# Kernel tuning notes

Measured on AMD Instinct MI355X. Metric: run time of the kernel, lower is better.

## Reference

```python
import jax, jax.numpy as jnp
import numpy as np
import math

B, C, H, W = 32, 3, 512, 512
K = 16
OUT_H, OUT_W = 512, 512

def _ctrl_pts(k):
    gs = int(math.sqrt(k))
    lin = jnp.linspace(-1.0, 1.0, gs)
    gy, gx = jnp.meshgrid(lin, lin, indexing='ij')
    return jnp.stack([gx, gy], axis=-1).reshape(-1, 2)

def setup_inputs() -> dict:
    key = jax.random.key(0)
    k1, k2, k3, k4 = jax.random.split(key, 4)
    x = jax.random.normal(k1, (B, C, H, W), jnp.float32)
    conv_w = jax.random.normal(k2, (8, C, 7, 7), jnp.float32) * 0.05
    conv_b = jax.random.normal(k3, (8,), jnp.float32) * 0.05
    fc_w = jax.random.normal(k4, (2 * K, 8), jnp.float32) * 0.01
    fc_b = jnp.asarray(_ctrl_pts(K).reshape(-1))  # module inits bias to ctrl grid
    return {"x": x, "conv_w": conv_w, "conv_b": conv_b, "fc_w": fc_w, "fc_b": fc_b}

def _U(sq):
    # U(r) = r^2 * log(r^2 + 1e-6), expressed with squared distance sq = r^2
    return sq * jnp.log(sq + 1e-6)

def _tps_grid(src, tgt, out_h, out_w):
    # src: [K,2] shared across batch (fixed ctrl grid), tgt: [B,K,2]
    Bb, Kk, _ = tgt.shape
    lin_y = jnp.linspace(-1.0, 1.0, out_h)
    lin_x = jnp.linspace(-1.0, 1.0, out_w)
    gy, gx = jnp.meshgrid(lin_y, lin_x, indexing='ij')
    grid = jnp.stack([gx, gy], axis=-1).reshape(-1, 2)  # [N,2]
    N = out_h * out_w
    # RBF kernel between output grid and source ctrl pts: [N,K]
    d2 = jnp.sum((grid[:, None, :] - src[None, :, :]) ** 2, axis=-1)
    U = _U(d2)
    # TPS system matrix L [K+3,K+3]; src is batch-shared so build it once
    src_d2 = jnp.sum((src[:, None, :] - src[None, :, :]) ** 2, axis=-1)
    P = jnp.concatenate([jnp.ones((Kk, 1)), src], axis=1)  # [K,3]
    L = jnp.zeros((Kk + 3, Kk + 3))
    L = L.at[:Kk, :Kk].set(_U(src_d2))
    L = L.at[:Kk, Kk:].set(P)
    L = L.at[Kk:, :Kk].set(P.T)
    Y = jnp.concatenate([tgt, jnp.zeros((Bb, 3, 2))], axis=1)  # [B,K+3,2]
    Wmat = jnp.linalg.solve(L[None], Y)  # [B,K+3,2]
    Pg = jnp.concatenate([jnp.ones((N, 1)), grid], axis=1)  # [N,3]
    mapped = (jnp.einsum('nk,bkc->bnc', U, Wmat[:, :Kk])
              + jnp.einsum('np,bpc->bnc', Pg, Wmat[:, Kk:]))
    return mapped.reshape(Bb, out_h, out_w, 2)

def _grid_sample(x, grid):
    # bilinear, zero padding, align_corners=False (torch defaults)
    Bb, Cc, Hh, Ww = x.shape
    ix = ((grid[..., 0] + 1.0) * Ww - 1.0) * 0.5
    iy = ((grid[..., 1] + 1.0) * Hh - 1.0) * 0.5
    x0 = jnp.floor(ix)
    y0 = jnp.floor(iy)
    wx1 = ix - x0
    wy1 = iy - y0
    x0i = x0.astype(jnp.int32)
    y0i = y0.astype(jnp.int32)

    def gather(img, yy, xx):
        valid = ((yy >= 0) & (yy < Hh) & (xx >= 0) & (xx < Ww)).astype(img.dtype)
        yc = jnp.clip(yy, 0, Hh - 1)
        xc = jnp.clip(xx, 0, Ww - 1)
        return img[:, yc, xc] * valid[None]

    def per(img, x0i, y0i, wx1, wy1):
        wx0 = 1.0 - wx1
        wy0 = 1.0 - wy1
        v00 = gather(img, y0i, x0i)
        v01 = gather(img, y0i, x0i + 1)
        v10 = gather(img, y0i + 1, x0i)
        v11 = gather(img, y0i + 1, x0i + 1)
        return (v00 * (wy0 * wx0)[None] + v01 * (wy0 * wx1)[None]
                + v10 * (wy1 * wx0)[None] + v11 * (wy1 * wx1)[None])

    return jax.vmap(per)(x, x0i, y0i, wx1, wy1)

def reference(x, conv_w, conv_b, fc_w, fc_b):
    # localization: conv7x7 -> relu -> global avg pool -> fc
    feat = jax.lax.conv_general_dilated(
        x, conv_w, window_strides=(1, 1), padding='VALID',
        dimension_numbers=('NCHW', 'OIHW', 'NCHW'))
    feat = jax.nn.relu(feat + conv_b[None, :, None, None])
    pooled = feat.mean(axis=(2, 3))  # [B,8] (AdaptiveAvgPool2d(1))
    pred = (pooled @ fc_w.T + fc_b).reshape(-1, K, 2)  # [B,K,2]
    src = _ctrl_pts(K)
    grid = _tps_grid(src, pred, OUT_H, OUT_W)  # [B,OUT_H,OUT_W,2]
    return _grid_sample(x, grid)
```

## Files before the change

kernel.cpp:

```cpp
#include <hip/hip_runtime.h>
#include <hip/hip_bf16.h>
#include <hip/hip_fp16.h>
#include <math.h>

#define BATCH 32
#define CH_IN 3
#define CH_OUT 8
#define IMG 512
#define KSZ 7
#define CONV_OUT 506
#define KPTS 16
#define TILES_PER_B 128

#define SROWS 23
#define PITCH_DW 76
#define SMEM_DW (CH_IN * SROWS * PITCH_DW)

#define BPB 8

typedef _Float16 half8_t __attribute__((ext_vector_type(8)));
typedef float f32x4_t __attribute__((ext_vector_type(4)));

__device__ __forceinline__ unsigned short f2h_bits(float f) {
    _Float16 h = (_Float16)f;
    unsigned short u;
    __builtin_memcpy(&u, &h, 2);
    return u;
}
__device__ __forceinline__ float h2f_bits(unsigned short u) {
    _Float16 h;
    __builtin_memcpy(&h, &u, 2);
    return (float)h;
}

__global__ __launch_bounds__(256)
void h16_kernel(const float* __restrict__ x, unsigned int* __restrict__ xh) {
    const int total4 = BATCH * CH_IN * IMG * IMG / 4;
    int stride = gridDim.x * 256;
    for (int p = blockIdx.x * 256 + threadIdx.x; p < total4; p += stride) {
        float4 v = ((const float4*)x)[p];
        unsigned int lo = (unsigned int)f2h_bits(v.x) | ((unsigned int)f2h_bits(v.y) << 16);
        unsigned int hi = (unsigned int)f2h_bits(v.z) | ((unsigned int)f2h_bits(v.w) << 16);
        xh[2 * p] = lo;
        xh[2 * p + 1] = hi;
    }
}

__global__ void wprep_kernel(const float* __restrict__ w, uint4* __restrict__ afrag) {
    int idx = blockIdx.x * 256 + threadIdx.x;
    if (idx >= 6 * 64) return;
    int s = idx >> 6, l = idx & 63;
    int m = l & 15;
    int dlt = m >> 3, o = m & 7;
    int oct = s * 4 + (l >> 4);
    int c = oct >> 3, ky = oct & 7;
    unsigned short h[8];
    #pragma unroll
    for (int j = 0; j < 8; ++j) {
        int kx = j - dlt;
        float v = 0.f;
        if (ky < KSZ && kx >= 0 && kx < KSZ)
            v = w[((o * CH_IN + c) * KSZ + ky) * KSZ + kx];
        h[j] = f2h_bits(v);
    }
    uint4 out;
    __builtin_memcpy(&out, h, 16);
    afrag[idx] = out;
}

template <bool H16>
__global__ __launch_bounds__(256)
void conv_pool_kernel(const float* __restrict__ x, const unsigned short* __restrict__ xh,
                      const uint4* __restrict__ afrag, const float* __restrict__ conv_b,
                      float* __restrict__ partial) {
    __shared__ unsigned int smem[SMEM_DW];
    __shared__ float red[4][8];

    int blk = blockIdx.x;
    int b = blk >> 7;
    int stripe = (blk >> 2) & 31;
    int chunk = blk & 3;
    int ybase = stripe * 16;
    int x0 = chunk * 128;
    int tid = threadIdx.x;

    if (H16) {
        const unsigned short* xhb = xh + (size_t)b * CH_IN * IMG * IMG;
        for (int idx4 = tid; idx4 < SMEM_DW / 4; idx4 += 256) {
            int c = idx4 / (SROWS * 19);
            int rem = idx4 - c * (SROWS * 19);
            int r = rem / 19;
            int u4 = rem - r * 19;
            int grow = ybase + r;
            int gcol = x0 + (u4 << 3);
            uint4 v = make_uint4(0u, 0u, 0u, 0u);
            if (grow < IMG) {
                const unsigned short* rp = xhb + ((size_t)c * IMG + grow) * IMG;
                if (gcol + 8 <= IMG) {
                    v = *(const uint4*)(rp + gcol);
                } else {
                    unsigned short h[8] = {0, 0, 0, 0, 0, 0, 0, 0};
                    #pragma unroll
                    for (int j = 0; j < 8; ++j) {
                        int cc = gcol + j;
                        if (cc < IMG) h[j] = rp[cc];
                    }
                    __builtin_memcpy(&v, h, 16);
                }
            }
            ((uint4*)smem)[idx4] = v;
        }
    } else {
        for (int idx = tid; idx < SMEM_DW; idx += 256) {
            int c = idx / (SROWS * PITCH_DW);
            int rem = idx - c * (SROWS * PITCH_DW);
            int r = rem / PITCH_DW;
            int u = rem - r * PITCH_DW;
            int grow = ybase + r, gcol = x0 + 2 * u;
            float f0 = 0.f, f1 = 0.f;
            if (grow < IMG) {
                const float* rp = x + (((size_t)b * CH_IN + c) * IMG + grow) * IMG;
                if (gcol < IMG) f0 = rp[gcol];
                if (gcol + 1 < IMG) f1 = rp[gcol + 1];
            }
            smem[idx] = (unsigned int)f2h_bits(f0) | ((unsigned int)f2h_bits(f1) << 16);
        }
    }
    __syncthreads();

    int l = tid & 63, w = tid >> 6;
    int n = l & 15, g = l >> 4;

    uint4 at[6];
    #pragma unroll
    for (int s = 0; s < 6; ++s) at[s] = afrag[s * 64 + l];

    int rowb[6];
    #pragma unroll
    for (int s = 0; s < 6; ++s) {
        int oct = s * 4 + g;
        int c = oct >> 3, ky = oct & 7;
        rowb[s] = (c * SROWS + n + ky) * (PITCH_DW * 4) + w * 64;
    }

    float bias_[4];
    {
        int ob = (g & 1) * 4;
        #pragma unroll
        for (int r2 = 0; r2 < 4; ++r2) bias_[r2] = conv_b[ob + r2];
    }
    bool rowok = (ybase + n) < CONV_OUT;
    int dlt = g >> 1;
    float sums[4] = {0.f, 0.f, 0.f, 0.f};
    const char* sb = (const char*)smem;

    #pragma unroll
    for (int u = 0; u < 4; ++u) {
        f32x4_t acc[4];
        #pragma unroll
        for (int d = 0; d < 4; ++d) acc[d] = (f32x4_t){0.f, 0.f, 0.f, 0.f};

        #pragma unroll
        for (int s = 0; s < 6; ++s) {
            uint4 lo = *(const uint4*)(sb + rowb[s] + (u << 4));
            uint4 hi = *(const uint4*)(sb + rowb[s] + (u << 4) + 16);
            unsigned int eu[8] = {lo.x, lo.y, lo.z, lo.w, hi.x, hi.y, hi.z, hi.w};
            half8_t a;
            __builtin_memcpy(&a, &at[s], 16);
            #pragma unroll
            for (int d = 0; d < 4; ++d) {
                uint4 bu = make_uint4(eu[d], eu[d + 1], eu[d + 2], eu[d + 3]);
                half8_t bf;
                __builtin_memcpy(&bf, &bu, 16);
                acc[d] = __builtin_amdgcn_mfma_f32_16x16x32_f16(a, bf, acc[d], 0, 0, 0);
            }
        }

        #pragma unroll
        for (int d = 0; d < 4; ++d) {
            int col = x0 + 32 * w + 8 * u + 2 * d + dlt;
            bool colok = col < CONV_OUT;
            #pragma unroll
            for (int r2 = 0; r2 < 4; ++r2) {
                float v = acc[d][r2] + bias_[r2];
                v = v > 0.f ? v : 0.f;
                sums[r2] += (rowok && colok) ? v : 0.f;
            }
        }
    }

    #pragma unroll
    for (int r2 = 0; r2 < 4; ++r2) {
        sums[r2] += __shfl_xor(sums[r2], 1, 64);
        sums[r2] += __shfl_xor(sums[r2], 2, 64);
        sums[r2] += __shfl_xor(sums[r2], 4, 64);
        sums[r2] += __shfl_xor(sums[r2], 8, 64);
        sums[r2] += __shfl_xor(sums[r2], 32, 64);
    }
    if (l == 0) {
        #pragma unroll
        for (int r2 = 0; r2 < 4; ++r2) red[w][r2] = sums[r2];
    }
    if (l == 16) {
        #pragma unroll
        for (int r2 = 0; r2 < 4; ++r2) red[w][4 + r2] = sums[r2];
    }
    __syncthreads();
    if (tid < CH_OUT) {
        float s = red[0][tid] + red[1][tid] + red[2][tid] + red[3][tid];
        partial[(b * TILES_PER_B + stripe * 4 + chunk) * CH_OUT + tid] = s;
    }
}

__device__ __forceinline__ double ctrl_lin(int i) { return -1.0 + (2.0 / 3.0) * i; }

__global__ void solve_kernel(const float* __restrict__ partial,
                             const float* __restrict__ fc_w,
                             const float* __restrict__ fc_b,
                             float* __restrict__ Wf) {
    __shared__ double L[19][19];
    __shared__ double Ys[19][64];
    __shared__ double piv_fac[19];
    __shared__ int piv_idx;
    __shared__ float pooledS[BATCH][CH_OUT];

    int t = threadIdx.x;

    for (int p = t; p < BATCH * CH_OUT; p += 64) {
        int b = p >> 3, o = p & 7;
        double s = 0.0;
        for (int tt = 0; tt < TILES_PER_B; ++tt)
            s += (double)partial[(b * TILES_PER_B + tt) * CH_OUT + o];
        pooledS[b][o] = (float)(s / ((double)CONV_OUT * (double)CONV_OUT));
    }
    __syncthreads();

    {
        int b = t >> 1, c = t & 1;
        for (int k = 0; k < KPTS; ++k) {
            int j = k * 2 + c;
            double s = (double)fc_b[j];
            for (int o = 0; o < CH_OUT; ++o)
                s += (double)pooledS[b][o] * (double)fc_w[j * CH_OUT + o];
            Ys[k][t] = s;
        }
        for (int k = KPTS; k < 19; ++k) Ys[k][t] = 0.0;
    }

    for (int p = t; p < 19 * 19; p += 64) {
        int r = p / 19, cc = p % 19;
        double v;
        if (r < KPTS && cc < KPTS) {
            double dx = ctrl_lin(r & 3) - ctrl_lin(cc & 3);
            double dy = ctrl_lin(r >> 2) - ctrl_lin(cc >> 2);
            double d2 = dx * dx + dy * dy;
            v = d2 * log(d2 + 1e-6);
        } else if (r < KPTS) {
            v = (cc == KPTS) ? 1.0 : (cc == KPTS + 1 ? ctrl_lin(r & 3) : ctrl_lin(r >> 2));
        } else if (cc < KPTS) {
            v = (r == KPTS) ? 1.0 : (r == KPTS + 1 ? ctrl_lin(cc & 3) : ctrl_lin(cc >> 2));
        } else v = 0.0;
        L[r][cc] = v;
    }
    __syncthreads();

    for (int k = 0; k < 19; ++k) {
        if (t == 0) {
            int pi = k; double mx = fabs(L[k][k]);
            for (int i = k + 1; i < 19; ++i) {
                double a = fabs(L[i][k]);
                if (a > mx) { mx = a; pi = i; }
            }
            piv_idx = pi;
        }
        __syncthreads();
        int pi = piv_idx;
        if (pi != k) {
            if (t < 19) { double tmp = L[k][t]; L[k][t] = L[pi][t]; L[pi][t] = tmp; }
            { double tmp = Ys[k][t]; Ys[k][t] = Ys[pi][t]; Ys[pi][t] = tmp; }
        }
        __syncthreads();
        if (t > k && t < 19) piv_fac[t] = L[t][k] / L[k][k];
        __syncthreads();
        if (t > k && t < 19) {
            double lkj = L[k][t];
            for (int i = k + 1; i < 19; ++i) L[i][t] -= piv_fac[i] * lkj;
        }
        {
            double ykt = Ys[k][t];
            for (int i = k + 1; i < 19; ++i) Ys[i][t] -= piv_fac[i] * ykt;
        }
        __syncthreads();
    }

    for (int k = 18; k >= 0; --k) {
        double s = Ys[k][t];
        for (int j = k + 1; j < 19; ++j) s -= L[k][j] * Ys[j][t];
        Ys[k][t] = s / L[k][k];
    }

    {
        int b = t >> 1, c = t & 1;
        for (int k = 0; k < 19; ++k)
            Wf[(b * 19 + k) * 2 + c] = (float)Ys[k][t];
    }
}

template <bool H16>
__global__ __launch_bounds__(256)
void tps_sample_kernel(const float* __restrict__ x, const unsigned short* __restrict__ xh,
                       const float* __restrict__ Wf, float* __restrict__ out) {
    int blk = blockIdx.x;
    int bgrp = blk >> 10;
    int pix = ((blk & 1023) << 8) | threadIdx.x;
    int i = pix >> 9, j = pix & 511;

    float gx = -1.f + (2.f / 511.f) * (float)j;
    float gy = -1.f + (2.f / 511.f) * (float)i;

    float U[KPTS];
    #pragma unroll
    for (int k = 0; k < KPTS; ++k) {
        float sx = -1.f + (2.f / 3.f) * (float)(k & 3);
        float sy = -1.f + (2.f / 3.f) * (float)(k >> 2);
        float dx = gx - sx, dy = gy - sy;
        float d2 = dx * dx + dy * dy;
        U[k] = d2 * (0.69314718055994531f * __log2f(d2 + 1e-6f));
    }

    for (int b = bgrp * BPB; b < bgrp * BPB + BPB; ++b) {
        const float* Wb = Wf + b * 38;

        float mx = Wb[32] + gx * Wb[34] + gy * Wb[36];
        float my = Wb[33] + gx * Wb[35] + gy * Wb[37];
        #pragma unroll
        for (int k = 0; k < KPTS; ++k) {
            mx += U[k] * Wb[2 * k];
            my += U[k] * Wb[2 * k + 1];
        }

        float ix = (mx + 1.f) * 256.f - 0.5f;
        float iy = (my + 1.f) * 256.f - 0.5f;
        float x0f = floorf(ix), y0f = floorf(iy);
        int x0 = (int)x0f, y0 = (int)y0f;
        int x1 = x0 + 1, y1 = y0 + 1;
        float wx1 = ix - x0f, wy1 = iy - y0f;
        float wx0 = 1.f - wx1, wy0 = 1.f - wy1;

        bool vx0 = (x0 >= 0) & (x0 < IMG), vx1 = (x1 >= 0) & (x1 < IMG);
        bool vy0 = (y0 >= 0) & (y0 < IMG), vy1 = (y1 >= 0) & (y1 < IMG);
        int xc0 = min(max(x0, 0), IMG - 1), xc1 = min(max(x1, 0), IMG - 1);
        int yc0 = min(max(y0, 0), IMG - 1), yc1 = min(max(y1, 0), IMG - 1);

        float w00 = (vy0 && vx0) ? wy0 * wx0 : 0.f;
        float w01 = (vy0 && vx1) ? wy0 * wx1 : 0.f;
        float w10 = (vy1 && vx0) ? wy1 * wx0 : 0.f;
        float w11 = (vy1 && vx1) ? wy1 * wx1 : 0.f;

        int o00 = yc0 * IMG + xc0, o01 = yc0 * IMG + xc1;
        int o10 = yc1 * IMG + xc0, o11 = yc1 * IMG + xc1;

        #pragma unroll
        for (int c = 0; c < CH_IN; ++c) {
            float v;
            if (H16) {
                const unsigned short* xp = xh + ((size_t)b * CH_IN + c) * IMG * IMG;
                v = h2f_bits(xp[o00]) * w00 + h2f_bits(xp[o01]) * w01
                  + h2f_bits(xp[o10]) * w10 + h2f_bits(xp[o11]) * w11;
            } else {
                const float* xp = x + ((size_t)b * CH_IN + c) * IMG * IMG;
                v = xp[o00] * w00 + xp[o01] * w01 + xp[o10] * w10 + xp[o11] * w11;
            }
            out[(((size_t)b * CH_IN + c) << 18) + (i << 9) + j] = v;
        }
    }
}

extern "C" void kernel_launch(void* const* d_in, const int* in_sizes, int n_in,
                              void* d_out, int out_size, void* d_ws, size_t ws_size,
                              hipStream_t stream) {
    const float* x      = (const float*)d_in[0];
    const float* conv_w = (const float*)d_in[1];
    const float* conv_b = (const float*)d_in[2];
    const float* fc_w   = (const float*)d_in[3];
    const float* fc_b   = (const float*)d_in[4];
    float* out = (float*)d_out;

    char* ws = (char*)d_ws;
    uint4* afrag   = (uint4*)ws;
    float* partial = (float*)(ws + 8192);
    float* Wf      = (float*)(ws + 139264);
    unsigned short* xh = (unsigned short*)(ws + 147456);
    const size_t need = 147456 + (size_t)BATCH * CH_IN * IMG * IMG * 2;
    bool useH16 = ws_size >= need;

    wprep_kernel<<<dim3(2), dim3(256), 0, stream>>>(conv_w, afrag);
    if (useH16) {
        h16_kernel<<<dim3(4096), dim3(256), 0, stream>>>(x, (unsigned int*)xh);
        conv_pool_kernel<true><<<dim3(BATCH * TILES_PER_B), dim3(256), 0, stream>>>(
            x, xh, afrag, conv_b, partial);
    } else {
        conv_pool_kernel<false><<<dim3(BATCH * TILES_PER_B), dim3(256), 0, stream>>>(
            x, xh, afrag, conv_b, partial);
    }
    solve_kernel<<<dim3(1), dim3(64), 0, stream>>>(partial, fc_w, fc_b, Wf);
    if (useH16) {
        tps_sample_kernel<true><<<dim3(4 * 1024), dim3(256), 0, stream>>>(x, xh, Wf, out);
    } else {
        tps_sample_kernel<false><<<dim3(4 * 1024), dim3(256), 0, stream>>>(x, xh, Wf, out);
    }
}
```

Before: 162.8 us.

## Fuse fp16 image conversion into conv-pool tile loads and transpose partial sums

Drops the separate fp32-to-fp16 conversion kernel. The conv-pool kernel now reads fp32 tiles directly, packs them to fp16 in shared memory, and writes each tile's owned 16x128 region to the fp16 copy that the sampling kernel uses. This removes one full pass over the input and a kernel launch, at the cost of reading fp32 halo rows in the conv kernel. The partial-sum layout is also transposed so the solve kernel can reduce with contiguous float4 loads and four accumulators.

Result: faster. 145.5 us (-10.6%).

```diff
diff --git a/kernel.cpp b/kernel.cpp
--- a/kernel.cpp
+++ b/kernel.cpp
@@ -32,18 +32,8 @@
     __builtin_memcpy(&h, &u, 2);
     return (float)h;
 }
-
-__global__ __launch_bounds__(256)
-void h16_kernel(const float* __restrict__ x, unsigned int* __restrict__ xh) {
-    const int total4 = BATCH * CH_IN * IMG * IMG / 4;
-    int stride = gridDim.x * 256;
-    for (int p = blockIdx.x * 256 + threadIdx.x; p < total4; p += stride) {
-        float4 v = ((const float4*)x)[p];
-        unsigned int lo = (unsigned int)f2h_bits(v.x) | ((unsigned int)f2h_bits(v.y) << 16);
-        unsigned int hi = (unsigned int)f2h_bits(v.z) | ((unsigned int)f2h_bits(v.w) << 16);
-        xh[2 * p] = lo;
-        xh[2 * p + 1] = hi;
-    }
+__device__ __forceinline__ unsigned int pk2(float a, float b) {
+    return (unsigned int)f2h_bits(a) | ((unsigned int)f2h_bits(b) << 16);
 }
 
 __global__ void wprep_kernel(const float* __restrict__ w, uint4* __restrict__ afrag) {
@@ -68,9 +58,9 @@
     afrag[idx] = out;
 }
 
-template <bool H16>
+template <bool FUSED>
 __global__ __launch_bounds__(256)
-void conv_pool_kernel(const float* __restrict__ x, const unsigned short* __restrict__ xh,
+void conv_pool_kernel(const float* __restrict__ x, unsigned short* __restrict__ xh,
                       const uint4* __restrict__ afrag, const float* __restrict__ conv_b,
                       float* __restrict__ partial) {
     __shared__ unsigned int smem[SMEM_DW];
@@ -84,8 +74,9 @@
     int x0 = chunk * 128;
     int tid = threadIdx.x;
 
-    if (H16) {
-        const unsigned short* xhb = xh + (size_t)b * CH_IN * IMG * IMG;
+    if (FUSED) {
+        const float* xb = x + (size_t)b * CH_IN * IMG * IMG;
+        unsigned short* xhb = xh + (size_t)b * CH_IN * IMG * IMG;
         for (int idx4 = tid; idx4 < SMEM_DW / 4; idx4 += 256) {
             int c = idx4 / (SROWS * 19);
             int rem = idx4 - c * (SROWS * 19);
@@ -94,21 +85,18 @@
             int grow = ybase + r;
             int gcol = x0 + (u4 << 3);
             uint4 v = make_uint4(0u, 0u, 0u, 0u);
-            if (grow < IMG) {
-                const unsigned short* rp = xhb + ((size_t)c * IMG + grow) * IMG;
-                if (gcol + 8 <= IMG) {
-                    v = *(const uint4*)(rp + gcol);
-                } else {
-                    unsigned short h[8] = {0, 0, 0, 0, 0, 0, 0, 0};
-                    #pragma unroll
-                    for (int j = 0; j < 8; ++j) {
-                        int cc = gcol + j;
-                        if (cc < IMG) h[j] = rp[cc];
-                    }
-                    __builtin_memcpy(&v, h, 16);
-                }
+            if (grow < IMG && gcol < IMG) {
+                const float* rp = xb + ((size_t)c * IMG + grow) * IMG + gcol;
+                float4 f0 = *(const float4*)rp;
+                float4 f1 = *(const float4*)(rp + 4);
+                v.x = pk2(f0.x, f0.y);
+                v.y = pk2(f0.z, f0.w);
+                v.z = pk2(f1.x, f1.y);
+                v.w = pk2(f1.z, f1.w);
             }
             ((uint4*)smem)[idx4] = v;
+            if (r < 16 && u4 < 16)
+                *(uint4*)(xhb + ((size_t)c * IMG + grow) * IMG + gcol) = v;
         }
     } else {
         for (int idx = tid; idx < SMEM_DW; idx += 256) {
@@ -123,7 +111,7 @@
                 if (gcol < IMG) f0 = rp[gcol];
                 if (gcol + 1 < IMG) f1 = rp[gcol + 1];
             }
-            smem[idx] = (unsigned int)f2h_bits(f0) | ((unsigned int)f2h_bits(f1) << 16);
+            smem[idx] = pk2(f0, f1);
         }
     }
     __syncthreads();
@@ -208,7 +196,7 @@
     __syncthreads();
     if (tid < CH_OUT) {
         float s = red[0][tid] + red[1][tid] + red[2][tid] + red[3][tid];
-        partial[(b * TILES_PER_B + stripe * 4 + chunk) * CH_OUT + tid] = s;
+        partial[tid * (BATCH * TILES_PER_B) + b * TILES_PER_B + stripe * 4 + chunk] = s;
     }
 }
 
@@ -228,10 +216,15 @@
 
     for (int p = t; p < BATCH * CH_OUT; p += 64) {
         int b = p >> 3, o = p & 7;
-        double s = 0.0;
-        for (int tt = 0; tt < TILES_PER_B; ++tt)
-            s += (double)partial[(b * TILES_PER_B + tt) * CH_OUT + o];
-        pooledS[b][o] = (float)(s / ((double)CONV_OUT * (double)CONV_OUT));
+        const float4* pp = (const float4*)(partial + o * (BATCH * TILES_PER_B) + b * TILES_PER_B);
+        double a0 = 0.0, a1 = 0.0, a2 = 0.0, a3 = 0.0;
+        #pragma unroll
+        for (int gq = 0; gq < TILES_PER_B / 4; ++gq) {
+            float4 v = pp[gq];
+            a0 += (double)v.x; a1 += (double)v.y;
+            a2 += (double)v.z; a3 += (double)v.w;
+        }
+        pooledS[b][o] = (float)(((a0 + a1) + (a2 + a3)) / ((double)CONV_OUT * (double)CONV_OUT));
     }
     __syncthreads();
 
@@ -392,11 +385,10 @@
     float* Wf      = (float*)(ws + 139264);
     unsigned short* xh = (unsigned short*)(ws + 147456);
     const size_t need = 147456 + (size_t)BATCH * CH_IN * IMG * IMG * 2;
-    bool useH16 = ws_size >= need;
+    bool fused = ws_size >= need;
 
     wprep_kernel<<<dim3(2), dim3(256), 0, stream>>>(conv_w, afrag);
-    if (useH16) {
-        h16_kernel<<<dim3(4096), dim3(256), 0, stream>>>(x, (unsigned int*)xh);
+    if (fused) {
         conv_pool_kernel<true><<<dim3(BATCH * TILES_PER_B), dim3(256), 0, stream>>>(
             x, xh, afrag, conv_b, partial);
     } else {
@@ -404,7 +396,7 @@
             x, xh, afrag, conv_b, partial);
     }
     solve_kernel<<<dim3(1), dim3(64), 0, stream>>>(partial, fc_w, fc_b, Wf);
-    if (useH16) {
+    if (fused) {
         tps_sample_kernel<true><<<dim3(4 * 1024), dim3(256), 0, stream>>>(x, xh, Wf, out);
     } else {
         tps_sample_kernel<false><<<dim3(4 * 1024), dim3(256), 0, stream>>>(x, xh, Wf, out);
```
